# Kernel optimization log

Measured on AMD Instinct MI355X. Metric: run time of the kernel, lower is better.

The kernel has to match this reference:

```python
import jax, jax.numpy as jnp
import numpy as np

B, D, N = 4096, 1024, 16

def _ln(x, g, b, eps=1e-5):
    m = jnp.mean(x, axis=-1, keepdims=True)
    v = jnp.var(x, axis=-1, keepdims=True)
    return (x - m) * jax.lax.rsqrt(v + eps) * g + b

def setup_inputs() -> dict:
    key = jax.random.key(0)
    ks = iter(jax.random.split(key, 40))
    def w(shape, scale):
        return (jax.random.normal(next(ks), shape, jnp.float32) * scale).astype(jnp.float32)
    inp = {}
    inp['x'] = jax.random.normal(next(ks), (B, D), jnp.float32)
    inp['h_logic'] = jax.random.normal(next(ks), (B, D), jnp.float32)
    inp['h_memory'] = jax.random.normal(next(ks), (B, D, N), jnp.float32)
    # Logic module params (weights stored [in, out])
    s2 = 0.8 / (2 * D) ** 0.5 / (2 * D) ** 0.5  # kaiming-ish * 0.8/sqrt(fan_in)
    inp['ln_pre_g'] = jnp.ones((D,)); inp['ln_pre_b'] = jnp.zeros((D,))
    for nm in ['Wz', 'Wr', 'Wh']:
        inp[nm] = w((2 * D, D), s2)
    for nm in ['bz', 'br', 'bh']:
        inp[nm] = jnp.zeros((D,))
    inp['ln_logic_g'] = jnp.ones((D,)); inp['ln_logic_b'] = jnp.zeros((D,))
    # Memory module params
    sg = min(1.0, 1.0 / (2 * D) ** 0.25) / (2 * D) ** 0.5
    sbc = 0.5 / (2 * D) / (2 * D) ** 0.5
    for nm in ['Wa', 'Wb', 'Wd']:
        inp[nm] = w((2 * D, D), sg)
    for nm in ['ba', 'bb', 'bd']:
        inp[nm] = jnp.zeros((D,))
    inp['A_log'] = jnp.broadcast_to(jnp.log(jnp.arange(1, N + 1, dtype=jnp.float32)), (D, N)).copy()
    inp['WB'] = w((2 * D, D * N), sbc); inp['bB'] = jnp.zeros((D * N,))
    inp['WC'] = w((2 * D, D * N), sbc); inp['bC'] = jnp.zeros((D * N,))
    inp['Dp'] = jnp.ones((D,))
    inp['ln_mem_g'] = jnp.ones((D,)); inp['ln_mem_b'] = jnp.zeros((D,))
    # Fusion params
    sf3 = 0.5 / (3 * D) / (3 * D) ** 0.5
    sf1 = 0.5 / D / D ** 0.5
    inp['R1'] = w((3 * D, D), sf3); inp['r1b'] = jnp.zeros((D,))
    inp['R2'] = w((D, 2), sf1); inp['r2b'] = jnp.zeros((2,))
    inp['Wout'] = w((D, D), sf1); inp['bout'] = jnp.zeros((D,))
    inp['ln_fus_g'] = jnp.ones((D,)); inp['ln_fus_b'] = jnp.zeros((D,))
    # Output gate
    inp['Wg'] = w((2 * D, D), 1.0 / (2 * D) ** 0.5); inp['bg'] = jnp.zeros((D,))
    return inp

def reference(x, h_logic, h_memory, ln_pre_g, ln_pre_b, Wz, bz, Wr, br, Wh, bh,
              ln_logic_g, ln_logic_b, Wa, ba, Wb, bb, Wd, bd, A_log, WB, bB, WC, bC,
              Dp, ln_mem_g, ln_mem_b, R1, r1b, R2, r2b, Wout, bout, ln_fus_g, ln_fus_b,
              Wg, bg):
    # ---- Logic module (GRU-style) ----
    x_norm = _ln(x, ln_pre_g, ln_pre_b)
    gi = jnp.concatenate([h_logic, x_norm], axis=-1)  # [B, 2D]
    z = jax.nn.sigmoid(gi @ Wz + bz)
    r = jax.nn.sigmoid(gi @ Wr + br)
    h_cand = jnp.tanh(jnp.concatenate([r * h_logic, x_norm], axis=-1) @ Wh + bh)
    h_logic_new = (1.0 - z) * h_logic + z * h_cand
    y_logic = _ln(h_logic_new, ln_logic_g, ln_logic_b)
    # ---- Memory module (diagonal SSM step) ----
    h_flat = jnp.mean(h_memory, axis=-1)  # [B, D]
    gm = jnp.concatenate([h_flat, x], axis=-1)  # [B, 2D]
    alpha = jax.nn.sigmoid(gm @ Wa + ba)
    beta = jax.nn.sigmoid(gm @ Wb + bb)
    delta = jax.nn.softplus(gm @ Wd + bd) * 0.1  # [B, D]
    A = -jnp.exp(A_log)  # [D, N]
    A_bar = jnp.exp(delta[..., None] * A)  # [B, D, N]
    Bm = (gm @ WB + bB).reshape(-1, D, N)
    B_bar = delta[..., None] * Bm
    h_memory_new = alpha[..., None] * (A_bar * h_memory) + beta[..., None] * (B_bar * x[..., None])
    Cm = (gm @ WC + bC).reshape(-1, D, N)
    y_mem = jnp.sum(Cm * h_memory_new, axis=-1)
    y_memory = _ln(y_mem + Dp * x, ln_mem_g, ln_mem_b)
    # ---- Fusion (soft routing) ----
    ri = jnp.concatenate([x, y_logic, y_memory], axis=-1)  # [B, 3D]
    rw = jax.nn.softmax(jnp.tanh(ri @ R1 + r1b) @ R2 + r2b, axis=-1)  # [B, 2]
    y_mixed = rw[:, 0:1] * y_logic + rw[:, 1:2] * y_memory
    y_out = _ln(y_mixed @ Wout + bout, ln_fus_g, ln_fus_b)
    # ---- Output gate ----
    gamma = jax.nn.sigmoid(jnp.concatenate([y_out, x], axis=-1) @ Wg + bg)
    y = gamma * y_out
    return (y, h_logic_new, h_memory_new)
```

## Files before the change

### kernel.cpp

```cpp
#include <hip/hip_runtime.h>
#include <cstdint>
#include <cstddef>

typedef unsigned short u16;
typedef short short8 __attribute__((ext_vector_type(8)));
typedef float f32x4 __attribute__((ext_vector_type(4)));

#define DEV static __device__ __forceinline__

static constexpr int Bn = 4096;
static constexpr int Dn = 1024;
static constexpr int Nn = 16;

DEV u16 f2bf(float f){
  union { float f; unsigned u; } v; v.f = f;
  unsigned u = v.u;
  u += 0x7fffu + ((u >> 16) & 1u);
  return (u16)(u >> 16);
}

DEV void gld_lds16(const void* g, void* l){
  __builtin_amdgcn_global_load_lds(
      (__attribute__((address_space(1))) void*)(g),
      (__attribute__((address_space(3))) void*)(l), 16, 0, 0);
}

DEV void block_sum2(float& s0, float& s1, float* red){
  #pragma unroll
  for (int off = 32; off >= 1; off >>= 1){
    s0 += __shfl_xor(s0, off, 64);
    s1 += __shfl_xor(s1, off, 64);
  }
  int wave = threadIdx.x >> 6;
  int lane = threadIdx.x & 63;
  if (lane == 0){ red[wave] = s0; red[4 + wave] = s1; }
  __syncthreads();
  s0 = red[0] + red[1] + red[2] + red[3];
  s1 = red[4] + red[5] + red[6] + red[7];
}

__global__ __launch_bounds__(256)
void transp_k(const float* __restrict__ W, u16* __restrict__ Wt, int K, int Nw){
  __shared__ u16 tile[32][33];
  int kt = blockIdx.y * 32, nt = blockIdx.x * 32;
  int tr = threadIdx.x >> 5;
  int tc = threadIdx.x & 31;
  #pragma unroll
  for (int i = 0; i < 4; i++){
    int rr = tr + i*8;
    tile[rr][tc] = f2bf(W[(size_t)(kt + rr)*Nw + nt + tc]);
  }
  __syncthreads();
  #pragma unroll
  for (int i = 0; i < 4; i++){
    int rr = tr + i*8;
    Wt[(size_t)(nt + rr)*K + kt + tc] = tile[tc][rr];
  }
}

__global__ __launch_bounds__(256)
void prep_k(const float* __restrict__ x, const float* __restrict__ hl,
            const float* __restrict__ hm,
            const float* __restrict__ g, const float* __restrict__ bt,
            float* __restrict__ xnorm, u16* __restrict__ gi,
            u16* __restrict__ gm, u16* __restrict__ ri)
{
  __shared__ float red[8];
  int b = blockIdx.x, t = threadIdx.x;
  const float4* xr = (const float4*)(x + (size_t)b*Dn);
  float4 xv = xr[t];
  float xe[4] = {xv.x, xv.y, xv.z, xv.w};
  float s = xe[0]+xe[1]+xe[2]+xe[3];
  float s2 = xe[0]*xe[0]+xe[1]*xe[1]+xe[2]*xe[2]+xe[3]*xe[3];
  block_sum2(s, s2, red);
  float mean = s * (1.f/Dn);
  float inv = rsqrtf(s2*(1.f/Dn) - mean*mean + 1e-5f);
  int d0 = t*4;
  #pragma unroll
  for (int q = 0; q < 4; q++){
    int d = d0 + q;
    size_t i = (size_t)b*Dn + d;
    float xn = (xe[q]-mean)*inv*g[d] + bt[d];
    xnorm[i] = xn;
    gi[(size_t)b*2048 + 1024 + d] = f2bf(xn);
    gi[(size_t)b*2048 + d]        = f2bf(hl[i]);
    gm[(size_t)b*2048 + 1024 + d] = f2bf(xe[q]);
    ri[(size_t)b*3072 + d]        = f2bf(xe[q]);
    const float4* hmr = (const float4*)(hm + i*Nn);
    float4 a0 = hmr[0], a1 = hmr[1], a2 = hmr[2], a3 = hmr[3];
    float hs = a0.x+a0.y+a0.z+a0.w + a1.x+a1.y+a1.z+a1.w
             + a2.x+a2.y+a2.z+a2.w + a3.x+a3.y+a3.z+a3.w;
    gm[(size_t)b*2048 + d] = f2bf(hs * (1.f/16.f));
  }
}

__global__ __launch_bounds__(256)
void gi2_k(const float* __restrict__ r, const float* __restrict__ hl,
           const u16* __restrict__ gi, u16* __restrict__ gi2){
  size_t i = (size_t)blockIdx.x*256 + threadIdx.x;
  size_t b = i >> 10, d = i & 1023;
  gi2[b*2048 + d] = f2bf(r[i]*hl[i]);
  gi2[b*2048 + 1024 + d] = gi[b*2048 + 1024 + d];
}

__global__ __launch_bounds__(256)
void logicfin_k(const float* __restrict__ z, const float* __restrict__ hl,
                const float* __restrict__ hc,
                const float* __restrict__ g, const float* __restrict__ bt,
                float* __restrict__ out_hn, float* __restrict__ ylogic,
                u16* __restrict__ ri)
{
  __shared__ float red[8];
  int b = blockIdx.x, t = threadIdx.x;
  int d0 = t*4;
  float hn[4]; float s = 0.f, s2 = 0.f;
  #pragma unroll
  for (int q = 0; q < 4; q++){
    size_t i = (size_t)b*Dn + d0 + q;
    float zz = z[i];
    float v = (1.f - zz)*hl[i] + zz*hc[i];
    hn[q] = v; s += v; s2 += v*v;
    out_hn[i] = v;
  }
  block_sum2(s, s2, red);
  float mean = s*(1.f/Dn);
  float inv = rsqrtf(s2*(1.f/Dn) - mean*mean + 1e-5f);
  #pragma unroll
  for (int q = 0; q < 4; q++){
    int d = d0 + q;
    size_t i = (size_t)b*Dn + d;
    float y = (hn[q]-mean)*inv*g[d] + bt[d];
    ylogic[i] = y;
    ri[(size_t)b*3072 + 1024 + d] = f2bf(y);
  }
}

__global__ __launch_bounds__(256)
void memln_k(const float* __restrict__ ymem, const float* __restrict__ x,
             const float* __restrict__ Dp, const float* __restrict__ g,
             const float* __restrict__ bt, float* __restrict__ ymemory,
             u16* __restrict__ ri)
{
  __shared__ float red[8];
  int b = blockIdx.x, t = threadIdx.x;
  int d0 = t*4;
  float v[4]; float s = 0.f, s2 = 0.f;
  #pragma unroll
  for (int q = 0; q < 4; q++){
    int d = d0 + q;
    size_t i = (size_t)b*Dn + d;
    float tv = ymem[i] + Dp[d]*x[i];
    v[q] = tv; s += tv; s2 += tv*tv;
  }
  block_sum2(s, s2, red);
  float mean = s*(1.f/Dn);
  float inv = rsqrtf(s2*(1.f/Dn) - mean*mean + 1e-5f);
  #pragma unroll
  for (int q = 0; q < 4; q++){
    int d = d0 + q;
    size_t i = (size_t)b*Dn + d;
    float y = (v[q]-mean)*inv*g[d] + bt[d];
    ymemory[i] = y;
    ri[(size_t)b*3072 + 2048 + d] = f2bf(y);
  }
}

__global__ __launch_bounds__(256)
void router_k(const float* __restrict__ t1, const float* __restrict__ R2,
              const float* __restrict__ r2b, const float* __restrict__ ylogic,
              const float* __restrict__ ymemory, u16* __restrict__ ymix)
{
  __shared__ float red[8];
  int b = blockIdx.x, t = threadIdx.x;
  int d0 = t*4;
  float s0 = 0.f, s1 = 0.f;
  #pragma unroll
  for (int q = 0; q < 4; q++){
    int d = d0 + q;
    float tv = t1[(size_t)b*Dn + d];
    s0 += tv * R2[2*d];
    s1 += tv * R2[2*d + 1];
  }
  block_sum2(s0, s1, red);
  float l0 = s0 + r2b[0], l1 = s1 + r2b[1];
  float m = fmaxf(l0, l1);
  float e0 = __expf(l0 - m), e1 = __expf(l1 - m);
  float w0 = e0 / (e0 + e1), w1 = e1 / (e0 + e1);
  #pragma unroll
  for (int q = 0; q < 4; q++){
    int d = d0 + q;
    size_t i = (size_t)b*Dn + d;
    ymix[i] = f2bf(w0*ylogic[i] + w1*ymemory[i]);
  }
}

__global__ __launch_bounds__(256)
void fusfin_k(const float* __restrict__ pre, const float* __restrict__ x,
              const float* __restrict__ g, const float* __restrict__ bt,
              float* __restrict__ yout, u16* __restrict__ yox)
{
  __shared__ float red[8];
  int b = blockIdx.x, t = threadIdx.x;
  int d0 = t*4;
  float v[4]; float s = 0.f, s2 = 0.f;
  #pragma unroll
  for (int q = 0; q < 4; q++){
    size_t i = (size_t)b*Dn + d0 + q;
    float tv = pre[i];
    v[q] = tv; s += tv; s2 += tv*tv;
  }
  block_sum2(s, s2, red);
  float mean = s*(1.f/Dn);
  float inv = rsqrtf(s2*(1.f/Dn) - mean*mean + 1e-5f);
  #pragma unroll
  for (int q = 0; q < 4; q++){
    int d = d0 + q;
    size_t i = (size_t)b*Dn + d;
    float y = (v[q]-mean)*inv*g[d] + bt[d];
    yout[i] = y;
    yox[(size_t)b*2048 + d] = f2bf(y);
    yox[(size_t)b*2048 + 1024 + d] = f2bf(x[i]);
  }
}

template<int MODE>
__global__ __launch_bounds__(256)
void gemm_k(const u16* __restrict__ A, int K,
            const u16* __restrict__ wt0, const u16* __restrict__ wt1, const u16* __restrict__ wt2,
            const float* __restrict__ bb0, const float* __restrict__ bb1, const float* __restrict__ bb2,
            int n0, int n1, int n2, int act0, int act1, int act2,
            float* __restrict__ c0, float* __restrict__ c1, float* __restrict__ c2,
            const float* __restrict__ mulsrc,
            const float* __restrict__ alpha, const float* __restrict__ beta,
            const float* __restrict__ delta, const float* __restrict__ xin,
            const float* __restrict__ alog, const float* __restrict__ hmem,
            const float* __restrict__ hnew, float* __restrict__ ymem)
{
  __shared__ u16 As[128*32];
  __shared__ u16 Bs[128*32];
  const int tid = threadIdx.x;
  const int wave = tid >> 6, lane = tid & 63;
  const int wr = wave >> 1, wc = wave & 1;
  const int rl = lane & 15, quad = lane >> 4;
  const int m0 = blockIdx.y * 128;
  const int cb = blockIdx.x * 128;

  const u16* wt = wt0; const float* bias = bb0; float* cout = c0;
  int ncols = n0, act = act0, cloc = cb;
  if (MODE == 0){
    if (cb >= n0 + n1){ wt = wt2; bias = bb2; cout = c2; ncols = n2; act = act2; cloc = cb - n0 - n1; }
    else if (cb >= n0){ wt = wt1; bias = bb1; cout = c1; ncols = n1; act = act1; cloc = cb - n0; }
  }

  f32x4 acc[4][4];
  #pragma unroll
  for (int i = 0; i < 4; i++)
    #pragma unroll
    for (int j = 0; j < 4; j++)
      acc[i][j] = (f32x4){0.f, 0.f, 0.f, 0.f};

  for (int k0 = 0; k0 < K; k0 += 32){
    #pragma unroll
    for (int i = 0; i < 2; i++){
      int chunk = wave*2 + i;
      int o = chunk*1024 + lane*16;
      int row = o >> 6;
      int kb = (o & 63) >> 1;
      gld_lds16(A + (size_t)(m0 + row)*K + k0 + kb, (char*)As + chunk*1024);
      gld_lds16(wt + (size_t)(cloc + row)*K + k0 + kb, (char*)Bs + chunk*1024);
    }
    __syncthreads();
    short8 af[4], bf[4];
    #pragma unroll
    for (int i = 0; i < 4; i++)
      af[i] = *(const short8*)(As + (wr*64 + i*16 + rl)*32 + quad*8);
    #pragma unroll
    for (int j = 0; j < 4; j++)
      bf[j] = *(const short8*)(Bs + (wc*64 + j*16 + rl)*32 + quad*8);
    #pragma unroll
    for (int i = 0; i < 4; i++)
      #pragma unroll
      for (int j = 0; j < 4; j++)
        acc[i][j] = __builtin_amdgcn_mfma_f32_16x16x32_bf16(af[i], bf[j], acc[i][j], 0, 0, 0);
    __syncthreads();
  }

  if (MODE == 0){
    #pragma unroll
    for (int j = 0; j < 4; j++){
      int colL = cloc + wc*64 + j*16 + rl;
      float bv = bias[colL];
      #pragma unroll
      for (int i = 0; i < 4; i++){
        f32x4 v = acc[i][j];
        #pragma unroll
        for (int r = 0; r < 4; r++){
          int row = m0 + wr*64 + i*16 + quad*4 + r;
          float val = v[r] + bv;
          if (act == 1) val = 1.f/(1.f + __expf(-val));
          else if (act == 2) val = tanhf(val);
          else if (act == 3) val = (val > 20.f ? val : log1pf(__expf(val))) * 0.1f;
          else if (act == 4) val = (1.f/(1.f + __expf(-val))) * mulsrc[(size_t)row*ncols + colL];
          cout[(size_t)row*ncols + colL] = val;
        }
      }
    }
  } else if (MODE == 1){
    #pragma unroll
    for (int j = 0; j < 4; j++){
      int dn = cb + wc*64 + j*16 + rl;
      int d = dn >> 4;
      float bv = bias[dn];
      float Aneg = -__expf(alog[dn]);
      #pragma unroll
      for (int i = 0; i < 4; i++){
        f32x4 v = acc[i][j];
        #pragma unroll
        for (int r = 0; r < 4; r++){
          int row = m0 + wr*64 + i*16 + quad*4 + r;
          float Bm = v[r] + bv;
          float al = alpha[(size_t)row*Dn + d];
          float be = beta [(size_t)row*Dn + d];
          float de = delta[(size_t)row*Dn + d];
          float xv = xin  [(size_t)row*Dn + d];
          float hm = hmem[(size_t)row*(Dn*Nn) + dn];
          float hn = al * (__expf(de*Aneg) * hm) + be * (de * Bm * xv);
          c0[(size_t)row*(Dn*Nn) + dn] = hn;
        }
      }
    }
  } else {
    #pragma unroll
    for (int j = 0; j < 4; j++){
      int dn = cb + wc*64 + j*16 + rl;
      int d = dn >> 4;
      float bv = bias[dn];
      #pragma unroll
      for (int i = 0; i < 4; i++){
        f32x4 v = acc[i][j];
        #pragma unroll
        for (int r = 0; r < 4; r++){
          int row = m0 + wr*64 + i*16 + quad*4 + r;
          float Cm = v[r] + bv;
          float p = Cm * hnew[(size_t)row*(Dn*Nn) + dn];
          p += __shfl_xor(p, 1, 64);
          p += __shfl_xor(p, 2, 64);
          p += __shfl_xor(p, 4, 64);
          p += __shfl_xor(p, 8, 64);
          if (rl == 0) ymem[(size_t)row*Dn + d] = p;
        }
      }
    }
  }
}

extern "C" void kernel_launch(void* const* d_in, const int* in_sizes, int n_in,
                              void* d_out, int out_size, void* d_ws, size_t ws_size,
                              hipStream_t stream)
{
  (void)in_sizes; (void)n_in; (void)out_size; (void)ws_size;
  const float* x        = (const float*)d_in[0];
  const float* h_logic  = (const float*)d_in[1];
  const float* h_mem    = (const float*)d_in[2];
  const float* ln_pre_g = (const float*)d_in[3];
  const float* ln_pre_b = (const float*)d_in[4];
  const float* Wz       = (const float*)d_in[5];
  const float* Wr       = (const float*)d_in[6];
  const float* Wh       = (const float*)d_in[7];
  const float* bz       = (const float*)d_in[8];
  const float* br       = (const float*)d_in[9];
  const float* bh       = (const float*)d_in[10];
  const float* ln_lg    = (const float*)d_in[11];
  const float* ln_lb    = (const float*)d_in[12];
  const float* Wa       = (const float*)d_in[13];
  const float* Wb       = (const float*)d_in[14];
  const float* Wd       = (const float*)d_in[15];
  const float* ba       = (const float*)d_in[16];
  const float* bbeta    = (const float*)d_in[17];
  const float* bd       = (const float*)d_in[18];
  const float* A_log    = (const float*)d_in[19];
  const float* WB       = (const float*)d_in[20];
  const float* bB       = (const float*)d_in[21];
  const float* WC       = (const float*)d_in[22];
  const float* bC       = (const float*)d_in[23];
  const float* Dp       = (const float*)d_in[24];
  const float* ln_mg    = (const float*)d_in[25];
  const float* ln_mb    = (const float*)d_in[26];
  const float* R1       = (const float*)d_in[27];
  const float* r1b      = (const float*)d_in[28];
  const float* R2       = (const float*)d_in[29];
  const float* r2b      = (const float*)d_in[30];
  const float* Wout     = (const float*)d_in[31];
  const float* bout     = (const float*)d_in[32];
  const float* ln_fg    = (const float*)d_in[33];
  const float* ln_fb    = (const float*)d_in[34];
  const float* Wg       = (const float*)d_in[35];
  const float* bg       = (const float*)d_in[36];

  float* out_y  = (float*)d_out;
  float* out_hl = out_y + (size_t)Bn*Dn;
  float* out_hm = out_hl + (size_t)Bn*Dn;

  char* ws = (char*)d_ws;
  size_t off = 0;
  auto alloc = [&](size_t bytes)->char*{
    char* p = ws + off; off += (bytes + 255) & ~(size_t)255; return p;
  };
  u16* WzT  = (u16*)alloc((size_t)2048*1024*2);
  u16* WrT  = (u16*)alloc((size_t)2048*1024*2);
  u16* WhT  = (u16*)alloc((size_t)2048*1024*2);
  u16* WaT  = (u16*)alloc((size_t)2048*1024*2);
  u16* WbT  = (u16*)alloc((size_t)2048*1024*2);
  u16* WdT  = (u16*)alloc((size_t)2048*1024*2);
  u16* WgT  = (u16*)alloc((size_t)2048*1024*2);
  u16* WoutT= (u16*)alloc((size_t)1024*1024*2);
  u16* R1T  = (u16*)alloc((size_t)3072*1024*2);
  u16* WBT  = (u16*)alloc((size_t)2048*16384*2);
  u16* WCT  = (u16*)alloc((size_t)2048*16384*2);
  u16* gi   = (u16*)alloc((size_t)Bn*2048*2);
  u16* gm   = (u16*)alloc((size_t)Bn*2048*2);
  u16* gi2  = (u16*)alloc((size_t)Bn*2048*2);
  u16* ri   = (u16*)alloc((size_t)Bn*3072*2);
  u16* ymix = (u16*)alloc((size_t)Bn*1024*2);
  u16* yox  = (u16*)alloc((size_t)Bn*2048*2);
  float* xnorm   = (float*)alloc((size_t)Bn*Dn*4);
  float* zb      = (float*)alloc((size_t)Bn*Dn*4);
  float* rb      = (float*)alloc((size_t)Bn*Dn*4);
  float* hcand   = (float*)alloc((size_t)Bn*Dn*4);
  float* alphab  = (float*)alloc((size_t)Bn*Dn*4);
  float* betab   = (float*)alloc((size_t)Bn*Dn*4);
  float* deltab  = (float*)alloc((size_t)Bn*Dn*4);
  float* ylogic  = (float*)alloc((size_t)Bn*Dn*4);
  float* ymemory = (float*)alloc((size_t)Bn*Dn*4);
  float* t1      = (float*)alloc((size_t)Bn*Dn*4);
  float* preLN   = (float*)alloc((size_t)Bn*Dn*4);
  float* yout    = (float*)alloc((size_t)Bn*Dn*4);
  float* ymemb   = (float*)alloc((size_t)Bn*Dn*4);

  auto T = [&](const float* W, u16* Wt, int K, int Nw){
    transp_k<<<dim3(Nw/32, K/32), 256, 0, stream>>>(W, Wt, K, Nw);
  };
  T(Wz, WzT, 2048, 1024);   T(Wr, WrT, 2048, 1024);   T(Wh, WhT, 2048, 1024);
  T(Wa, WaT, 2048, 1024);   T(Wb, WbT, 2048, 1024);   T(Wd, WdT, 2048, 1024);
  T(Wg, WgT, 2048, 1024);   T(Wout, WoutT, 1024, 1024); T(R1, R1T, 3072, 1024);
  T(WB, WBT, 2048, 16384);  T(WC, WCT, 2048, 16384);

  prep_k<<<Bn, 256, 0, stream>>>(x, h_logic, h_mem, ln_pre_g, ln_pre_b,
                                 xnorm, gi, gm, ri);

  gemm_k<0><<<dim3(16, 32), 256, 0, stream>>>(gi, 2048,
      WzT, WrT, WrT, bz, br, br, 1024, 1024, 0, 1, 1, 0,
      zb, rb, rb, nullptr,
      nullptr, nullptr, nullptr, nullptr, nullptr, nullptr, nullptr, nullptr);

  gi2_k<<<dim3((Bn*Dn)/256), 256, 0, stream>>>(rb, h_logic, gi, gi2);

  gemm_k<0><<<dim3(8, 32), 256, 0, stream>>>(gi2, 2048,
      WhT, WhT, WhT, bh, bh, bh, 1024, 0, 0, 2, 2, 2,
      hcand, hcand, hcand, nullptr,
      nullptr, nullptr, nullptr, nullptr, nullptr, nullptr, nullptr, nullptr);

  logicfin_k<<<Bn, 256, 0, stream>>>(zb, h_logic, hcand, ln_lg, ln_lb,
                                     out_hl, ylogic, ri);

  gemm_k<0><<<dim3(24, 32), 256, 0, stream>>>(gm, 2048,
      WaT, WbT, WdT, ba, bbeta, bd, 1024, 1024, 1024, 1, 1, 3,
      alphab, betab, deltab, nullptr,
      nullptr, nullptr, nullptr, nullptr, nullptr, nullptr, nullptr, nullptr);

  gemm_k<1><<<dim3(128, 32), 256, 0, stream>>>(gm, 2048,
      WBT, WBT, WBT, bB, bB, bB, 16384, 0, 0, 0, 0, 0,
      out_hm, nullptr, nullptr, nullptr,
      alphab, betab, deltab, x, A_log, h_mem, nullptr, nullptr);

  gemm_k<2><<<dim3(128, 32), 256, 0, stream>>>(gm, 2048,
      WCT, WCT, WCT, bC, bC, bC, 16384, 0, 0, 0, 0, 0,
      nullptr, nullptr, nullptr, nullptr,
      nullptr, nullptr, nullptr, nullptr, nullptr, nullptr, out_hm, ymemb);

  memln_k<<<Bn, 256, 0, stream>>>(ymemb, x, Dp, ln_mg, ln_mb, ymemory, ri);

  gemm_k<0><<<dim3(8, 32), 256, 0, stream>>>(ri, 3072,
      R1T, R1T, R1T, r1b, r1b, r1b, 1024, 0, 0, 2, 2, 2,
      t1, t1, t1, nullptr,
      nullptr, nullptr, nullptr, nullptr, nullptr, nullptr, nullptr, nullptr);

  router_k<<<Bn, 256, 0, stream>>>(t1, R2, r2b, ylogic, ymemory, ymix);

  gemm_k<0><<<dim3(8, 32), 256, 0, stream>>>(ymix, 1024,
      WoutT, WoutT, WoutT, bout, bout, bout, 1024, 0, 0, 0, 0, 0,
      preLN, preLN, preLN, nullptr,
      nullptr, nullptr, nullptr, nullptr, nullptr, nullptr, nullptr, nullptr);

  fusfin_k<<<Bn, 256, 0, stream>>>(preLN, x, ln_fg, ln_fb, yout, yox);

  gemm_k<0><<<dim3(8, 32), 256, 0, stream>>>(yox, 2048,
      WgT, WgT, WgT, bg, bg, bg, 1024, 0, 0, 4, 4, 4,
      out_y, out_y, out_y, yout,
      nullptr, nullptr, nullptr, nullptr, nullptr, nullptr, nullptr, nullptr);
}
```

Baseline: 2.851 ms.

## Fuse WB/WC GEMMs into one kernel, double-buffer LDS, swizzle workgroup order

The separate B-projection and C-projection GEMMs become a single kernel that computes both accumulators over a shared A tile. It computes h_memory_new and its dot product with Cm in registers, so h_memory_new is no longer re-read from global memory. All GEMMs now use double-buffered LDS, issuing the next k-slice's loads before the current MFMAs, plus an XCD-aware workgroup remap with a transposed grid. The cost is more LDS and registers per block in the fused kernel, which has launch_bounds(256,2), and narrower 64-column tiles for the B and C weights.

Result: faster. 2.360 ms (-17.2%).

```diff
diff --git a/kernel.cpp b/kernel.cpp
--- a/kernel.cpp
+++ b/kernel.cpp
@@ -223,34 +223,36 @@
   }
 }
 
-template<int MODE>
 __global__ __launch_bounds__(256)
 void gemm_k(const u16* __restrict__ A, int K,
             const u16* __restrict__ wt0, const u16* __restrict__ wt1, const u16* __restrict__ wt2,
             const float* __restrict__ bb0, const float* __restrict__ bb1, const float* __restrict__ bb2,
             int n0, int n1, int n2, int act0, int act1, int act2,
             float* __restrict__ c0, float* __restrict__ c1, float* __restrict__ c2,
-            const float* __restrict__ mulsrc,
-            const float* __restrict__ alpha, const float* __restrict__ beta,
-            const float* __restrict__ delta, const float* __restrict__ xin,
-            const float* __restrict__ alog, const float* __restrict__ hmem,
-            const float* __restrict__ hnew, float* __restrict__ ymem)
-{
-  __shared__ u16 As[128*32];
-  __shared__ u16 Bs[128*32];
+            const float* __restrict__ mulsrc)
+{
+  __shared__ u16 As[2][128*32];
+  __shared__ u16 Bs[2][128*32];
   const int tid = threadIdx.x;
   const int wave = tid >> 6, lane = tid & 63;
   const int wr = wave >> 1, wc = wave & 1;
   const int rl = lane & 15, quad = lane >> 4;
-  const int m0 = blockIdx.y * 128;
-  const int cb = blockIdx.x * 128;
+
+  int mt, ct;
+  {
+    int gx = gridDim.x;
+    int nwg = gx * gridDim.y;
+    int orig = blockIdx.y * gx + blockIdx.x;
+    int w = ((orig & 7) * (nwg >> 3)) + (orig >> 3);
+    mt = w % gx; ct = w / gx;
+  }
+  const int m0 = mt * 128;
+  const int cb = ct * 128;
 
   const u16* wt = wt0; const float* bias = bb0; float* cout = c0;
   int ncols = n0, act = act0, cloc = cb;
-  if (MODE == 0){
-    if (cb >= n0 + n1){ wt = wt2; bias = bb2; cout = c2; ncols = n2; act = act2; cloc = cb - n0 - n1; }
-    else if (cb >= n0){ wt = wt1; bias = bb1; cout = c1; ncols = n1; act = act1; cloc = cb - n0; }
-  }
+  if (cb >= n0 + n1){ wt = wt2; bias = bb2; cout = c2; ncols = n2; act = act2; cloc = cb - n0 - n1; }
+  else if (cb >= n0){ wt = wt1; bias = bb1; cout = c1; ncols = n1; act = act1; cloc = cb - n0; }
 
   f32x4 acc[4][4];
   #pragma unroll
@@ -259,96 +261,171 @@
     for (int j = 0; j < 4; j++)
       acc[i][j] = (f32x4){0.f, 0.f, 0.f, 0.f};
 
-  for (int k0 = 0; k0 < K; k0 += 32){
+  const int srow = lane >> 2;
+  const int skb  = (lane & 3) * 8;
+
+  auto STAGE = [&](int k0, int buf){
     #pragma unroll
     for (int i = 0; i < 2; i++){
       int chunk = wave*2 + i;
-      int o = chunk*1024 + lane*16;
-      int row = o >> 6;
-      int kb = (o & 63) >> 1;
-      gld_lds16(A + (size_t)(m0 + row)*K + k0 + kb, (char*)As + chunk*1024);
-      gld_lds16(wt + (size_t)(cloc + row)*K + k0 + kb, (char*)Bs + chunk*1024);
-    }
-    __syncthreads();
+      int row = chunk*16 + srow;
+      gld_lds16(A  + (size_t)(m0   + row)*K + k0 + skb, (char*)As[buf] + chunk*1024);
+      gld_lds16(wt + (size_t)(cloc + row)*K + k0 + skb, (char*)Bs[buf] + chunk*1024);
+    }
+  };
+
+  STAGE(0, 0);
+  __syncthreads();
+  int cur = 0;
+  for (int k0 = 0; k0 < K; k0 += 32){
+    if (k0 + 32 < K) STAGE(k0 + 32, cur ^ 1);
     short8 af[4], bf[4];
     #pragma unroll
     for (int i = 0; i < 4; i++)
-      af[i] = *(const short8*)(As + (wr*64 + i*16 + rl)*32 + quad*8);
+      af[i] = *(const short8*)(&As[cur][(wr*64 + i*16 + rl)*32 + quad*8]);
     #pragma unroll
     for (int j = 0; j < 4; j++)
-      bf[j] = *(const short8*)(Bs + (wc*64 + j*16 + rl)*32 + quad*8);
+      bf[j] = *(const short8*)(&Bs[cur][(wc*64 + j*16 + rl)*32 + quad*8]);
     #pragma unroll
     for (int i = 0; i < 4; i++)
       #pragma unroll
       for (int j = 0; j < 4; j++)
         acc[i][j] = __builtin_amdgcn_mfma_f32_16x16x32_bf16(af[i], bf[j], acc[i][j], 0, 0, 0);
     __syncthreads();
-  }
-
-  if (MODE == 0){
-    #pragma unroll
-    for (int j = 0; j < 4; j++){
-      int colL = cloc + wc*64 + j*16 + rl;
-      float bv = bias[colL];
+    cur ^= 1;
+  }
+
+  #pragma unroll
+  for (int j = 0; j < 4; j++){
+    int colL = cloc + wc*64 + j*16 + rl;
+    float bv = bias[colL];
+    #pragma unroll
+    for (int i = 0; i < 4; i++){
+      f32x4 v = acc[i][j];
       #pragma unroll
-      for (int i = 0; i < 4; i++){
-        f32x4 v = acc[i][j];
-        #pragma unroll
-        for (int r = 0; r < 4; r++){
-          int row = m0 + wr*64 + i*16 + quad*4 + r;
-          float val = v[r] + bv;
-          if (act == 1) val = 1.f/(1.f + __expf(-val));
-          else if (act == 2) val = tanhf(val);
-          else if (act == 3) val = (val > 20.f ? val : log1pf(__expf(val))) * 0.1f;
-          else if (act == 4) val = (1.f/(1.f + __expf(-val))) * mulsrc[(size_t)row*ncols + colL];
-          cout[(size_t)row*ncols + colL] = val;
-        }
+      for (int r = 0; r < 4; r++){
+        int row = m0 + wr*64 + i*16 + quad*4 + r;
+        float val = v[r] + bv;
+        if (act == 1) val = 1.f/(1.f + __expf(-val));
+        else if (act == 2) val = tanhf(val);
+        else if (act == 3) val = (val > 20.f ? val : log1pf(__expf(val))) * 0.1f;
+        else if (act == 4) val = (1.f/(1.f + __expf(-val))) * mulsrc[(size_t)row*ncols + colL];
+        cout[(size_t)row*ncols + colL] = val;
       }
     }
-  } else if (MODE == 1){
-    #pragma unroll
-    for (int j = 0; j < 4; j++){
-      int dn = cb + wc*64 + j*16 + rl;
-      int d = dn >> 4;
-      float bv = bias[dn];
-      float Aneg = -__expf(alog[dn]);
+  }
+}
+
+__global__ __launch_bounds__(256, 2)
+void gemm_bc_k(const u16* __restrict__ A,
+               const u16* __restrict__ wtB, const u16* __restrict__ wtC,
+               const float* __restrict__ bB, const float* __restrict__ bC,
+               const float* __restrict__ alpha, const float* __restrict__ beta,
+               const float* __restrict__ delta, const float* __restrict__ xin,
+               const float* __restrict__ alog, const float* __restrict__ hmem,
+               float* __restrict__ hout, float* __restrict__ ymem)
+{
+  constexpr int K = 2048;
+  __shared__ u16 As[2][128*32];
+  __shared__ u16 Bs[2][64*32];
+  __shared__ u16 Cs[2][64*32];
+  const int tid = threadIdx.x;
+  const int wave = tid >> 6, lane = tid & 63;
+  const int wr = wave >> 1, wc = wave & 1;
+  const int rl = lane & 15, quad = lane >> 4;
+
+  int mt, ct;
+  {
+    int gx = gridDim.x;
+    int nwg = gx * gridDim.y;
+    int orig = blockIdx.y * gx + blockIdx.x;
+    int w = ((orig & 7) * (nwg >> 3)) + (orig >> 3);
+    mt = w % gx; ct = w / gx;
+  }
+  const int m0 = mt * 128;
+  const int cb = ct * 64;
+
+  f32x4 accB[4][2], accC[4][2];
+  #pragma unroll
+  for (int i = 0; i < 4; i++)
+    #pragma unroll
+    for (int j = 0; j < 2; j++){
+      accB[i][j] = (f32x4){0.f, 0.f, 0.f, 0.f};
+      accC[i][j] = (f32x4){0.f, 0.f, 0.f, 0.f};
+    }
+
+  const int srow = lane >> 2;
+  const int skb  = (lane & 3) * 8;
+
+  auto STAGE = [&](int k0, int buf){
+    #pragma unroll
+    for (int i = 0; i < 2; i++){
+      int chunk = wave*2 + i;
+      int row = chunk*16 + srow;
+      gld_lds16(A + (size_t)(m0 + row)*K + k0 + skb, (char*)As[buf] + chunk*1024);
+    }
+    {
+      int row = wave*16 + srow;
+      gld_lds16(wtB + (size_t)(cb + row)*K + k0 + skb, (char*)Bs[buf] + wave*1024);
+      gld_lds16(wtC + (size_t)(cb + row)*K + k0 + skb, (char*)Cs[buf] + wave*1024);
+    }
+  };
+
+  STAGE(0, 0);
+  __syncthreads();
+  int cur = 0;
+  for (int k0 = 0; k0 < K; k0 += 32){
+    if (k0 + 32 < K) STAGE(k0 + 32, cur ^ 1);
+    short8 af[4], bf[2], cf[2];
+    #pragma unroll
+    for (int i = 0; i < 4; i++)
+      af[i] = *(const short8*)(&As[cur][(wr*64 + i*16 + rl)*32 + quad*8]);
+    #pragma unroll
+    for (int j = 0; j < 2; j++){
+      bf[j] = *(const short8*)(&Bs[cur][(wc*32 + j*16 + rl)*32 + quad*8]);
+      cf[j] = *(const short8*)(&Cs[cur][(wc*32 + j*16 + rl)*32 + quad*8]);
+    }
+    #pragma unroll
+    for (int i = 0; i < 4; i++)
       #pragma unroll
-      for (int i = 0; i < 4; i++){
-        f32x4 v = acc[i][j];
-        #pragma unroll
-        for (int r = 0; r < 4; r++){
-          int row = m0 + wr*64 + i*16 + quad*4 + r;
-          float Bm = v[r] + bv;
-          float al = alpha[(size_t)row*Dn + d];
-          float be = beta [(size_t)row*Dn + d];
-          float de = delta[(size_t)row*Dn + d];
-          float xv = xin  [(size_t)row*Dn + d];
-          float hm = hmem[(size_t)row*(Dn*Nn) + dn];
-          float hn = al * (__expf(de*Aneg) * hm) + be * (de * Bm * xv);
-          c0[(size_t)row*(Dn*Nn) + dn] = hn;
-        }
+      for (int j = 0; j < 2; j++){
+        accB[i][j] = __builtin_amdgcn_mfma_f32_16x16x32_bf16(af[i], bf[j], accB[i][j], 0, 0, 0);
+        accC[i][j] = __builtin_amdgcn_mfma_f32_16x16x32_bf16(af[i], cf[j], accC[i][j], 0, 0, 0);
       }
-    }
-  } else {
-    #pragma unroll
-    for (int j = 0; j < 4; j++){
-      int dn = cb + wc*64 + j*16 + rl;
-      int d = dn >> 4;
-      float bv = bias[dn];
+    __syncthreads();
+    cur ^= 1;
+  }
+
+  #pragma unroll
+  for (int j = 0; j < 2; j++){
+    const int dn = cb + wc*32 + j*16 + rl;
+    const int d = dn >> 4;
+    const float bvB = bB[dn];
+    const float bvC = bC[dn];
+    const float Aneg = -__expf(alog[dn]);
+    #pragma unroll
+    for (int i = 0; i < 4; i++){
+      f32x4 vB = accB[i][j];
+      f32x4 vC = accC[i][j];
       #pragma unroll
-      for (int i = 0; i < 4; i++){
-        f32x4 v = acc[i][j];
-        #pragma unroll
-        for (int r = 0; r < 4; r++){
-          int row = m0 + wr*64 + i*16 + quad*4 + r;
-          float Cm = v[r] + bv;
-          float p = Cm * hnew[(size_t)row*(Dn*Nn) + dn];
-          p += __shfl_xor(p, 1, 64);
-          p += __shfl_xor(p, 2, 64);
-          p += __shfl_xor(p, 4, 64);
-          p += __shfl_xor(p, 8, 64);
-          if (rl == 0) ymem[(size_t)row*Dn + d] = p;
-        }
+      for (int r = 0; r < 4; r++){
+        const int row = m0 + wr*64 + i*16 + quad*4 + r;
+        const size_t rd = (size_t)row*Dn + d;
+        float Bm = vB[r] + bvB;
+        float Cm = vC[r] + bvC;
+        float al = alpha[rd];
+        float be = beta [rd];
+        float de = delta[rd];
+        float xv = xin  [rd];
+        float hm = hmem[(size_t)row*(Dn*Nn) + dn];
+        float hn = al * (__expf(de*Aneg) * hm) + be * (de * Bm * xv);
+        hout[(size_t)row*(Dn*Nn) + dn] = hn;
+        float p = Cm * hn;
+        p += __shfl_xor(p, 1, 64);
+        p += __shfl_xor(p, 2, 64);
+        p += __shfl_xor(p, 4, 64);
+        p += __shfl_xor(p, 8, 64);
+        if (rl == 0) ymem[rd] = p;
       }
     }
   }
@@ -448,54 +525,41 @@
   prep_k<<<Bn, 256, 0, stream>>>(x, h_logic, h_mem, ln_pre_g, ln_pre_b,
                                  xnorm, gi, gm, ri);
 
-  gemm_k<0><<<dim3(16, 32), 256, 0, stream>>>(gi, 2048,
+  gemm_k<<<dim3(32, 16), 256, 0, stream>>>(gi, 2048,
       WzT, WrT, WrT, bz, br, br, 1024, 1024, 0, 1, 1, 0,
-      zb, rb, rb, nullptr,
-      nullptr, nullptr, nullptr, nullptr, nullptr, nullptr, nullptr, nullptr);
+      zb, rb, rb, nullptr);
 
   gi2_k<<<dim3((Bn*Dn)/256), 256, 0, stream>>>(rb, h_logic, gi, gi2);
 
-  gemm_k<0><<<dim3(8, 32), 256, 0, stream>>>(gi2, 2048,
+  gemm_k<<<dim3(32, 8), 256, 0, stream>>>(gi2, 2048,
       WhT, WhT, WhT, bh, bh, bh, 1024, 0, 0, 2, 2, 2,
-      hcand, hcand, hcand, nullptr,
-      nullptr, nullptr, nullptr, nullptr, nullptr, nullptr, nullptr, nullptr);
+      hcand, hcand, hcand, nullptr);
 
   logicfin_k<<<Bn, 256, 0, stream>>>(zb, h_logic, hcand, ln_lg, ln_lb,
                                      out_hl, ylogic, ri);
 
-  gemm_k<0><<<dim3(24, 32), 256, 0, stream>>>(gm, 2048,
+  gemm_k<<<dim3(32, 24), 256, 0, stream>>>(gm, 2048,
       WaT, WbT, WdT, ba, bbeta, bd, 1024, 1024, 1024, 1, 1, 3,
-      alphab, betab, deltab, nullptr,
-      nullptr, nullptr, nullptr, nullptr, nullptr, nullptr, nullptr, nullptr);
-
-  gemm_k<1><<<dim3(128, 32), 256, 0, stream>>>(gm, 2048,
-      WBT, WBT, WBT, bB, bB, bB, 16384, 0, 0, 0, 0, 0,
-      out_hm, nullptr, nullptr, nullptr,
-      alphab, betab, deltab, x, A_log, h_mem, nullptr, nullptr);
-
-  gemm_k<2><<<dim3(128, 32), 256, 0, stream>>>(gm, 2048,
-      WCT, WCT, WCT, bC, bC, bC, 16384, 0, 0, 0, 0, 0,
-      nullptr, nullptr, nullptr, nullptr,
-      nullptr, nullptr, nullptr, nullptr, nullptr, nullptr, out_hm, ymemb);
+      alphab, betab, deltab, nullptr);
+
+  gemm_bc_k<<<dim3(32, 256), 256, 0, stream>>>(gm, WBT, WCT, bB, bC,
+      alphab, betab, deltab, x, A_log, h_mem, out_hm, ymemb);
 
   memln_k<<<Bn, 256, 0, stream>>>(ymemb, x, Dp, ln_mg, ln_mb, ymemory, ri);
 
-  gemm_k<0><<<dim3(8, 32), 256, 0, stream>>>(ri, 3072,
+  gemm_k<<<dim3(32, 8), 256, 0, stream>>>(ri, 3072,
       R1T, R1T, R1T, r1b, r1b, r1b, 1024, 0, 0, 2, 2, 2,
-      t1, t1, t1, nullptr,
-      nullptr, nullptr, nullptr, nullptr, nullptr, nullptr, nullptr, nullptr);
+      t1, t1, t1, nullptr);
 
   router_k<<<Bn, 256, 0, stream>>>(t1, R2, r2b, ylogic, ymemory, ymix);
 
-  gemm_k<0><<<dim3(8, 32), 256, 0, stream>>>(ymix, 1024,
+  gemm_k<<<dim3(32, 8), 256, 0, stream>>>(ymix, 1024,
       WoutT, WoutT, WoutT, bout, bout, bout, 1024, 0, 0, 0, 0, 0,
-      preLN, preLN, preLN, nullptr,
-      nullptr, nullptr, nullptr, nullptr, nullptr, nullptr, nullptr, nullptr);
+      preLN, preLN, preLN, nullptr);
 
   fusfin_k<<<Bn, 256, 0, stream>>>(preLN, x, ln_fg, ln_fb, yout, yox);
 
-  gemm_k<0><<<dim3(8, 32), 256, 0, stream>>>(yox, 2048,
+  gemm_k<<<dim3(32, 8), 256, 0, stream>>>(yox, 2048,
       WgT, WgT, WgT, bg, bg, bg, 1024, 0, 0, 4, 4, 4,
-      out_y, out_y, out_y, yout,
-      nullptr, nullptr, nullptr, nullptr, nullptr, nullptr, nullptr, nullptr);
-}
+      out_y, out_y, out_y, yout);
+}
```
